# Performance work log

Measured on AMD Instinct MI355X. Metric: run time of the kernel, lower is better.

The kernel has to match this reference:

```python
import jax, jax.numpy as jnp
import numpy as np

B, S, H = 4, 2048, 1024
NH = 1                     # source code only type-checks with 1 head (see notes)
DH = H // NH               # head dim == hidden size
DT = 32                    # distance_type
LN_EPS = 1e-12


def setup_inputs() -> dict:
    key = jax.random.key(0)
    ks = jax.random.split(key, 12)
    sd = 0.02
    hidden_states = jax.random.normal(ks[0], (B, S, H), dtype=jnp.float32)
    attention_mask = jnp.zeros((B, 1, 1, S), dtype=jnp.float32)
    word_word_relation = jax.random.randint(ks[1], (B, S, S), 0, DT, dtype=jnp.int64)
    dist_emb = sd * jax.random.normal(ks[2], (DT, H), dtype=jnp.float32)
    dist_emb = dist_emb.at[0].set(0.0)  # padding_idx=0
    return {
        "hidden_states": hidden_states,
        "attention_mask": attention_mask,
        "word_word_relation": word_word_relation,
        "Wq": sd * jax.random.normal(ks[3], (H, H), dtype=jnp.float32),
        "bq": jnp.zeros((H,), dtype=jnp.float32),
        "Wk": sd * jax.random.normal(ks[4], (H, H), dtype=jnp.float32),
        "bk": jnp.zeros((H,), dtype=jnp.float32),
        "Wv": sd * jax.random.normal(ks[5], (H, H), dtype=jnp.float32),
        "bv": jnp.zeros((H,), dtype=jnp.float32),
        "dist_emb": dist_emb,
        "Wo": sd * jax.random.normal(ks[6], (H, H), dtype=jnp.float32),
        "bo": jnp.zeros((H,), dtype=jnp.float32),
        "ln_g": jnp.ones((H,), dtype=jnp.float32),
        "ln_b": jnp.zeros((H,), dtype=jnp.float32),
    }


def _split_heads(x):
    # [B,S,H] -> [B,NH,S,DH]
    return x.reshape(B, S, NH, DH).transpose(0, 2, 1, 3)


def reference(hidden_states, attention_mask, word_word_relation, Wq, bq, Wk, bk,
              Wv, bv, dist_emb, Wo, bo, ln_g, ln_b):
    q = _split_heads(hidden_states @ Wq.T + bq)   # [B,NH,S,DH]
    k = _split_heads(hidden_states @ Wk.T + bk)
    v = _split_heads(hidden_states @ Wv.T + bv)

    # raw QK^T scores [B,NH,S,S]
    scores = jnp.einsum('bhqd,bhkd->bhqk', q, k)

    # query . distance_embedding^T : [B,NH,S,DT]
    word_dot_distance = jnp.einsum('bhqd,td->bhqt', q, dist_emb)

    rel = word_word_relation[:, None, :, :]       # [B,1,S,S]
    # gather per-pair distance score along the distance-type axis
    dist_att = jnp.take_along_axis(word_dot_distance, rel, axis=3)  # [B,NH,S,S]
    mask_out = (rel == 1).astype(scores.dtype)    # keep only relation==1 pairs
    dist_att = dist_att * mask_out

    scores = (scores + dist_att) / jnp.sqrt(jnp.asarray(DH, scores.dtype))
    scores = scores + attention_mask              # additive BERT mask
    probs = jax.nn.softmax(scores, axis=-1)       # dropout p=0 -> identity

    ctx = jnp.einsum('bhqk,bhkd->bhqd', probs, v) # [B,NH,S,DH]
    ctx = ctx.transpose(0, 2, 1, 3).reshape(B, S, H)

    # BertSelfOutput: dense -> residual -> LayerNorm
    attn_out = ctx @ Wo.T + bo
    x = attn_out + hidden_states
    mu = jnp.mean(x, axis=-1, keepdims=True)
    var = jnp.mean(jnp.square(x - mu), axis=-1, keepdims=True)
    out = (x - mu) * jax.lax.rsqrt(var + LN_EPS) * ln_g + ln_b
    return out
```

## Files before the change

### kernel.cpp

```cpp
#include <hip/hip_runtime.h>

#define BM 256
#define BN 128
#define BK 64
#define NBUF 3
#define BUFELEMS ((BM + BN) * BK)

typedef __bf16 bf16x8 __attribute__((ext_vector_type(8)));
typedef __bf16 bf16x4 __attribute__((ext_vector_type(4)));
typedef float f32x4 __attribute__((ext_vector_type(4)));
typedef __bf16 bf16_t;

#define MFMA16(a, b, c) __builtin_amdgcn_mfma_f32_16x16x32_bf16((a), (b), (c), 0, 0, 0)

__device__ __forceinline__ void gl_lds16(const void* g, void* l) {
    __builtin_amdgcn_global_load_lds(
        (const __attribute__((address_space(1))) void*)g,
        (__attribute__((address_space(3))) void*)l, 16, 0, 0);
}
__device__ __forceinline__ void barrier_mem() {
    asm volatile("s_barrier" ::: "memory");
}

__global__ __launch_bounds__(256)
void cvt_all_kernel(const float* __restrict__ hid,
                    const float* __restrict__ w0, const float* __restrict__ w1,
                    const float* __restrict__ w2, const float* __restrict__ w3,
                    bf16_t* __restrict__ hidb, bf16_t* __restrict__ wb)
{
    const int bid = blockIdx.x;
    const float* src;
    bf16_t* dst;
    size_t off;
    if (bid < 8192) {
        src = hid; dst = hidb; off = (size_t)bid * 1024;
    } else {
        const int i = (bid - 8192) >> 10;
        src = (i == 0) ? w0 : (i == 1) ? w1 : (i == 2) ? w2 : w3;
        dst = wb + (size_t)i * 1024 * 1024;
        off = (size_t)((bid - 8192) & 1023) * 1024;
    }
    const size_t idx = off + threadIdx.x * 4;
    const float4 v = *(const float4*)(src + idx);
    bf16x4 o;
    o[0] = (__bf16)v.x; o[1] = (__bf16)v.y;
    o[2] = (__bf16)v.z; o[3] = (__bf16)v.w;
    *(bf16x4*)(dst + idx) = o;
}

template <int MODE>
__global__ __launch_bounds__(512, 2)
void gemm_bt(const bf16_t* __restrict__ A, const bf16_t* __restrict__ Bw,
             const float* __restrict__ bias, const float* __restrict__ bias2,
             const float* __restrict__ bias3,
             bf16_t* __restrict__ C, bf16_t* __restrict__ C2,
             int M, int N, int K,
             long long sAz, long long sBz, long long sCz,
             const float* __restrict__ resid,
             int Sdim, int DHdim)
{
    const int bz = blockIdx.z;
    const float* bi = bias;
    if (MODE == 0) {
        Bw += (long long)bz * N * K;
        bi = (bz == 0) ? bias : (bz == 1 ? bias2 : bias3);
        if (bz < 2) C += (long long)bz * sCz;
    } else {
        A += (long long)bz * sAz;
        Bw += (long long)bz * sBz;
        C += (long long)bz * sCz;
    }
    const int num_n = N / BN;
    const int pid = blockIdx.x;
    const int group = 8 * num_n;
    const int g = pid / group;
    const int m0 = (g * 8 + (pid % 8)) * BM;
    const int n0 = ((pid % group) >> 3) * BN;

    const int tid = threadIdx.x;
    const int w = tid >> 6;
    const int lane = tid & 63;
    const int wr = w >> 1;
    const int wc = w & 1;
    const int frow = lane & 15;
    const int fchunk = lane >> 4;

    __shared__ bf16_t smem[NBUF * BUFELEMS];

    const int srow8 = lane >> 3;
    const int sch = (lane & 7) ^ srow8;
    const size_t soff = (size_t)(w * 8 + srow8) * K + ((size_t)sch << 3);
    const bf16_t* gA = A + (size_t)m0 * K;
    const bf16_t* gB = Bw + (size_t)n0 * K;

    auto stA = [&](int kt, int b, int i) {
        gl_lds16(gA + (size_t)(i * 64) * K + (size_t)kt * BK + soff,
                 smem + (size_t)b * BUFELEMS + (i * 64 + w * 8) * BK);
    };
    auto stB = [&](int kt, int b, int i) {
        gl_lds16(gB + (size_t)(i * 64) * K + (size_t)kt * BK + soff,
                 smem + (size_t)b * BUFELEMS + BM * BK + (i * 64 + w * 8) * BK);
    };

    f32x4 acc[4][4];
#pragma unroll
    for (int i = 0; i < 4; ++i)
#pragma unroll
        for (int j = 0; j < 4; ++j) acc[i][j] = (f32x4)0.0f;

    const int NT = K / BK;

#pragma unroll
    for (int i = 0; i < 4; ++i) stA(0, 0, i);
#pragma unroll
    for (int i = 0; i < 2; ++i) stB(0, 0, i);
#pragma unroll
    for (int i = 0; i < 4; ++i) stA(1, 1, i);
#pragma unroll
    for (int i = 0; i < 2; ++i) stB(1, 1, i);

    for (int kt = 0; kt < NT; ++kt) {
        const int cur = kt % NBUF;
        const int nxt = (kt + 2) % NBUF;
        const bool pf = (kt + 2 < NT);
        if (pf) { stA(kt + 2, nxt, 0); stA(kt + 2, nxt, 1); stA(kt + 2, nxt, 2); }
        if (pf)               asm volatile("s_waitcnt vmcnt(9)" ::: "memory");
        else if (kt + 1 < NT) asm volatile("s_waitcnt vmcnt(6)" ::: "memory");
        else                  asm volatile("s_waitcnt vmcnt(0)" ::: "memory");
        barrier_mem();

        const bf16_t* Ab = smem + (size_t)cur * BUFELEMS;
        const bf16_t* Bb = Ab + BM * BK;
        const int sw = frow & 7;

        bf16x8 af[4][2], b0v[2][2];
#pragma unroll
        for (int t = 0; t < 4; ++t) {
            const int row = wr * 64 + t * 16 + frow;
#pragma unroll
            for (int kh = 0; kh < 2; ++kh)
                af[t][kh] = *(const bf16x8*)&Ab[row * BK + (((kh * 4 + fchunk) ^ sw) << 3)];
        }
#pragma unroll
        for (int u = 0; u < 2; ++u) {
            const int row = wc * 64 + u * 16 + frow;
#pragma unroll
            for (int kh = 0; kh < 2; ++kh)
                b0v[u][kh] = *(const bf16x8*)&Bb[row * BK + (((kh * 4 + fchunk) ^ sw) << 3)];
        }
        if (pf) { stA(kt + 2, nxt, 3); stB(kt + 2, nxt, 0); stB(kt + 2, nxt, 1); }

        __builtin_amdgcn_s_setprio(1);
#pragma unroll
        for (int t = 0; t < 4; ++t)
#pragma unroll
            for (int u = 0; u < 2; ++u) {
                acc[t][u] = MFMA16(af[t][0], b0v[u][0], acc[t][u]);
                acc[t][u] = MFMA16(af[t][1], b0v[u][1], acc[t][u]);
            }
        __builtin_amdgcn_s_setprio(0);

        bf16x8 b1v[2][2];
#pragma unroll
        for (int u = 0; u < 2; ++u) {
            const int row = wc * 64 + (u + 2) * 16 + frow;
#pragma unroll
            for (int kh = 0; kh < 2; ++kh)
                b1v[u][kh] = *(const bf16x8*)&Bb[row * BK + (((kh * 4 + fchunk) ^ sw) << 3)];
        }
        barrier_mem();

        __builtin_amdgcn_s_setprio(1);
#pragma unroll
        for (int t = 0; t < 4; ++t)
#pragma unroll
            for (int u = 0; u < 2; ++u) {
                acc[t][u + 2] = MFMA16(af[t][0], b1v[u][0], acc[t][u + 2]);
                acc[t][u + 2] = MFMA16(af[t][1], b1v[u][1], acc[t][u + 2]);
            }
        __builtin_amdgcn_s_setprio(0);
        barrier_mem();
    }

    const int crow = (lane >> 4) * 4;
    const int ccol = lane & 15;

    if (MODE == 0 && bz == 2) {
#pragma unroll
        for (int mt = 0; mt < 4; ++mt) {
            const int mb = m0 + wr * 64 + mt * 16 + crow;
#pragma unroll
            for (int nt = 0; nt < 4; ++nt) {
                const int n = n0 + wc * 64 + nt * 16 + ccol;
                const float bvv = bi[n];
                const int b = mb >> 11;
                const int s = mb & 2047;
                union { ushort4 u; bf16_t h[4]; } pk;
#pragma unroll
                for (int r = 0; r < 4; ++r) pk.h[r] = (__bf16)(acc[mt][nt][r] + bvv);
                *(ushort4*)&C2[(size_t)b * DHdim * Sdim + (size_t)n * Sdim + s] = pk.u;
            }
        }
        return;
    }

    bf16_t* tw = smem + w * (16 * 72);
    const int r0 = lane >> 3;
    const int cseg = (lane & 7) * 8;

    float bv[4];
    if (MODE == 0 || MODE == 4) {
#pragma unroll
        for (int nt = 0; nt < 4; ++nt)
            bv[nt] = bi[n0 + wc * 64 + nt * 16 + ccol];
    }

#pragma unroll
    for (int mt = 0; mt < 4; ++mt) {
#pragma unroll
        for (int nt = 0; nt < 4; ++nt) {
            const float badd = (MODE == 0 || MODE == 4) ? bv[nt] : 0.0f;
#pragma unroll
            for (int r = 0; r < 4; ++r)
                tw[(crow + r) * 72 + nt * 16 + ccol] = (__bf16)(acc[mt][nt][r] + badd);
        }
        bf16x8 va = *(const bf16x8*)&tw[r0 * 72 + cseg];
        bf16x8 vb = *(const bf16x8*)&tw[(r0 + 8) * 72 + cseg];

        const int gm_a = m0 + wr * 64 + mt * 16 + r0;
        const int gm_b = gm_a + 8;
        const int gn = n0 + wc * 64 + cseg;

        if (MODE == 0 || MODE == 3) {
            *(bf16x8*)&C[(size_t)gm_a * N + gn] = va;
            *(bf16x8*)&C[(size_t)gm_b * N + gn] = vb;
        } else {
            const float4 xa0 = *(const float4*)&resid[(size_t)gm_a * N + gn];
            const float4 xa1 = *(const float4*)&resid[(size_t)gm_a * N + gn + 4];
            const float4 xb0 = *(const float4*)&resid[(size_t)gm_b * N + gn];
            const float4 xb1 = *(const float4*)&resid[(size_t)gm_b * N + gn + 4];
            bf16x8 oa, ob;
            oa[0] = (__bf16)((float)va[0] + xa0.x);
            oa[1] = (__bf16)((float)va[1] + xa0.y);
            oa[2] = (__bf16)((float)va[2] + xa0.z);
            oa[3] = (__bf16)((float)va[3] + xa0.w);
            oa[4] = (__bf16)((float)va[4] + xa1.x);
            oa[5] = (__bf16)((float)va[5] + xa1.y);
            oa[6] = (__bf16)((float)va[6] + xa1.z);
            oa[7] = (__bf16)((float)va[7] + xa1.w);
            ob[0] = (__bf16)((float)vb[0] + xb0.x);
            ob[1] = (__bf16)((float)vb[1] + xb0.y);
            ob[2] = (__bf16)((float)vb[2] + xb0.z);
            ob[3] = (__bf16)((float)vb[3] + xb0.w);
            ob[4] = (__bf16)((float)vb[4] + xb1.x);
            ob[5] = (__bf16)((float)vb[5] + xb1.y);
            ob[6] = (__bf16)((float)vb[6] + xb1.z);
            ob[7] = (__bf16)((float)vb[7] + xb1.w);
            *(bf16x8*)&C[(size_t)gm_a * N + gn] = oa;
            *(bf16x8*)&C[(size_t)gm_b * N + gn] = ob;
        }
    }
}

__global__ __launch_bounds__(256)
void softmax_kernel(bf16_t* __restrict__ sc, const int* __restrict__ rel,
                    const bf16_t* __restrict__ q, const float* __restrict__ de,
                    const float* __restrict__ mask)
{
    constexpr int S = 2048, H = 1024;
    const int row = blockIdx.x;
    const int b = row >> 11;
    const int tid = threadIdx.x;
    const int w = tid >> 6, lane = tid & 63;
    __shared__ float rd1[4], rmax[4], rsum[4];

    const bf16x4 q4 = *(const bf16x4*)(q + (size_t)row * H + tid * 4);
    const float4 e4 = *(const float4*)(de + H + tid * 4);
    float pd = (float)q4[0] * e4.x + (float)q4[1] * e4.y
             + (float)q4[2] * e4.z + (float)q4[3] * e4.w;
#pragma unroll
    for (int off = 32; off; off >>= 1) pd += __shfl_xor(pd, off, 64);
    if (lane == 0) rd1[w] = pd;
    __syncthreads();
    const float d1s = (rd1[0] + rd1[1] + rd1[2] + rd1[3]) * 0.03125f;

    bf16_t* p = sc + (size_t)row * S;
    const bf16x8 x = *(const bf16x8*)(p + tid * 8);
    const int4 rl0 = *(const int4*)&rel[(size_t)row * S + tid * 8];
    const int4 rl1 = *(const int4*)&rel[(size_t)row * S + tid * 8 + 4];
    const float4 mk0 = *(const float4*)&mask[(size_t)b * S + tid * 8];
    const float4 mk1 = *(const float4*)&mask[(size_t)b * S + tid * 8 + 4];
    const int rls[8] = {rl0.x, rl0.y, rl0.z, rl0.w, rl1.x, rl1.y, rl1.z, rl1.w};
    const float mks[8] = {mk0.x, mk0.y, mk0.z, mk0.w, mk1.x, mk1.y, mk1.z, mk1.w};
    float v[8];
    float mx = -1e30f;
#pragma unroll
    for (int j = 0; j < 8; ++j) {
        v[j] = (float)x[j] * 0.03125f + mks[j] + (rls[j] == 1 ? d1s : 0.0f);
        mx = fmaxf(mx, v[j]);
    }
#pragma unroll
    for (int off = 32; off; off >>= 1) mx = fmaxf(mx, __shfl_xor(mx, off, 64));
    if (lane == 0) rmax[w] = mx;
    __syncthreads();
    mx = fmaxf(fmaxf(rmax[0], rmax[1]), fmaxf(rmax[2], rmax[3]));
    float sum = 0.0f;
#pragma unroll
    for (int j = 0; j < 8; ++j) { v[j] = __expf(v[j] - mx); sum += v[j]; }
#pragma unroll
    for (int off = 32; off; off >>= 1) sum += __shfl_xor(sum, off, 64);
    if (lane == 0) rsum[w] = sum;
    __syncthreads();
    sum = rsum[0] + rsum[1] + rsum[2] + rsum[3];
    const float inv = 1.0f / sum;
    bf16x8 o;
#pragma unroll
    for (int j = 0; j < 8; ++j) o[j] = (__bf16)(v[j] * inv);
    *(bf16x8*)(p + tid * 8) = o;
}

__global__ __launch_bounds__(256)
void ln_kernel(const bf16_t* __restrict__ x, const float* __restrict__ gamma,
               const float* __restrict__ beta, float* __restrict__ out)
{
    const int H = 1024;
    const size_t row = blockIdx.x;
    const int tid = threadIdx.x;
    const int w = tid >> 6, lane = tid & 63;
    bf16x4 xv = *(const bf16x4*)(x + row * H + tid * 4);
    float v[4] = {(float)xv[0], (float)xv[1], (float)xv[2], (float)xv[3]};
    float s = 0.0f, s2 = 0.0f;
#pragma unroll
    for (int j = 0; j < 4; ++j) { s += v[j]; s2 += v[j] * v[j]; }
#pragma unroll
    for (int off = 32; off; off >>= 1) {
        s += __shfl_xor(s, off, 64);
        s2 += __shfl_xor(s2, off, 64);
    }
    __shared__ float rs[4], rs2[4];
    if (lane == 0) { rs[w] = s; rs2[w] = s2; }
    __syncthreads();
    s  = rs[0] + rs[1] + rs[2] + rs[3];
    s2 = rs2[0] + rs2[1] + rs2[2] + rs2[3];
    const float mu  = s * (1.0f / H);
    const float var = s2 * (1.0f / H) - mu * mu;
    const float inv = rsqrtf(var + 1e-12f);
    float4 o;
    const int c = tid * 4;
    o.x = (v[0] - mu) * inv * gamma[c + 0] + beta[c + 0];
    o.y = (v[1] - mu) * inv * gamma[c + 1] + beta[c + 1];
    o.z = (v[2] - mu) * inv * gamma[c + 2] + beta[c + 2];
    o.w = (v[3] - mu) * inv * gamma[c + 3] + beta[c + 3];
    *(float4*)(out + row * H + tid * 4) = o;
}

extern "C" void kernel_launch(void* const* d_in, const int* in_sizes, int n_in,
                              void* d_out, int out_size, void* d_ws, size_t ws_size,
                              hipStream_t stream)
{
    constexpr int B = 4, S = 2048, H = 1024;
    const float* hid = (const float*)d_in[0];
    const float* am  = (const float*)d_in[1];
    const int*   rel = (const int*)d_in[2];
    const float* Wq  = (const float*)d_in[3];
    const float* bq  = (const float*)d_in[4];
    const float* Wk  = (const float*)d_in[5];
    const float* bk  = (const float*)d_in[6];
    const float* Wv  = (const float*)d_in[7];
    const float* bv  = (const float*)d_in[8];
    const float* de  = (const float*)d_in[9];
    const float* Wo  = (const float*)d_in[10];
    const float* bo  = (const float*)d_in[11];
    const float* lng = (const float*)d_in[12];
    const float* lnb = (const float*)d_in[13];
    float* out = (float*)d_out;

    char* ws = (char*)d_ws;
    const int n_tok = B * S;
    const size_t MB = 1024 * 1024;
    bf16_t* hidb = (bf16_t*)(ws);
    bf16_t* Wqb  = (bf16_t*)(ws + 16 * MB);
    bf16_t* Wob  = (bf16_t*)(ws + 22 * MB);
    bf16_t* qb   = (bf16_t*)(ws + 24 * MB);
    bf16_t* kb   = (bf16_t*)(ws + 40 * MB);
    bf16_t* vT   = (bf16_t*)(ws + 56 * MB);
    bf16_t* ctx  = (bf16_t*)(ws + 72 * MB);
    bf16_t* sc   = (bf16_t*)(ws + 88 * MB);
    bf16_t* xb   = (bf16_t*)(ws + 88 * MB);

    const dim3 blk(256);
    const dim3 blkg(512);
    cvt_all_kernel<<<dim3(8192 + 4 * 1024), blk, 0, stream>>>(
        hid, Wq, Wk, Wv, Wo, hidb, Wqb);

    gemm_bt<0><<<dim3((n_tok / BM) * (H / BN), 1, 3), blkg, 0, stream>>>(
        hidb, Wqb, bq, bk, bv, qb, vT, n_tok, H, H,
        0, 0, (long long)n_tok * H,
        nullptr, S, H);
    gemm_bt<3><<<dim3((S / BM) * (S / BN), 1, B), blkg, 0, stream>>>(
        qb, kb, nullptr, nullptr, nullptr, sc, nullptr, S, S, H,
        (long long)S * H, (long long)S * H, (long long)S * S,
        nullptr, S, H);
    softmax_kernel<<<dim3(B * S), blk, 0, stream>>>(sc, rel, qb, de, am);
    gemm_bt<3><<<dim3((S / BM) * (H / BN), 1, B), blkg, 0, stream>>>(
        sc, vT, nullptr, nullptr, nullptr, ctx, nullptr, S, H, S,
        (long long)S * S, (long long)H * S, (long long)S * H,
        nullptr, S, H);
    gemm_bt<4><<<dim3((n_tok / BM) * (H / BN), 1, 1), blkg, 0, stream>>>(
        ctx, Wob, bo, nullptr, nullptr, xb, nullptr, n_tok, H, H, 0, 0, 0,
        hid, S, H);
    ln_kernel<<<dim3(n_tok), blk, 0, stream>>>(xb, lng, lnb, out);
}
```

Measured before the change: 335.5 us.

## Add 256x256-tile GEMM with 8-phase LDS pipeline for QKV and QK^T

Adds a new gemm8 kernel with 256x256 output tiles, each wave computing 128x64, double-buffered A/B LDS halves, and an 8-phase schedule that interleaves global-to-LDS loads with MFMA work. It also uses grouped block ordering for L2 reuse. The QKV projection and the QK^T score GEMM now use gemm8, while the remaining gemm_bt calls get split A-fragment loads and have their unused MODE 0 paths removed. The larger tiles cut global traffic per FLOP and reduce the number of blocks. The cost is higher register pressure from 128 accumulator floats per lane and fewer blocks, which may hurt occupancy and tail balance.

```diff
diff --git a/kernel.cpp b/kernel.cpp
--- a/kernel.cpp
+++ b/kernel.cpp
@@ -46,6 +46,190 @@
     o[0] = (__bf16)v.x; o[1] = (__bf16)v.y;
     o[2] = (__bf16)v.z; o[3] = (__bf16)v.w;
     *(bf16x4*)(dst + idx) = o;
+}
+
+#define PHASE(BUF, P, SG, SL, VM)                                            \
+  do {                                                                       \
+    bf16x8 a00 = rdA(BUF, 2 * (P), 0),     a01 = rdA(BUF, 2 * (P), 1);       \
+    bf16x8 a10 = rdA(BUF, 2 * (P) + 1, 0), a11 = rdA(BUF, 2 * (P) + 1, 1);   \
+    if ((P) == 0) {                                                          \
+      _Pragma("unroll")                                                      \
+      for (int nf = 0; nf < 4; ++nf) {                                       \
+        bfrag[nf][0] = rdB(BUF, nf, 0);                                      \
+        bfrag[nf][1] = rdB(BUF, nf, 1);                                      \
+      }                                                                      \
+    }                                                                        \
+    if (SG) {                                                                \
+      gl_lds16((SG) + soff,                   (SL) + (w << 9));              \
+      gl_lds16((SG) + soff + (size_t)64 * K,  (SL) + 4096 + (w << 9));       \
+    }                                                                        \
+    barrier_mem();                                                           \
+    asm volatile("s_waitcnt lgkmcnt(0)" ::: "memory");                       \
+    __builtin_amdgcn_s_setprio(1);                                           \
+    _Pragma("unroll")                                                        \
+    for (int nf = 0; nf < 4; ++nf) {                                         \
+      acc[2 * (P)][nf]     = MFMA16(a00, bfrag[nf][0], acc[2 * (P)][nf]);    \
+      acc[2 * (P)][nf]     = MFMA16(a01, bfrag[nf][1], acc[2 * (P)][nf]);    \
+      acc[2 * (P) + 1][nf] = MFMA16(a10, bfrag[nf][0], acc[2 * (P) + 1][nf]);\
+      acc[2 * (P) + 1][nf] = MFMA16(a11, bfrag[nf][1], acc[2 * (P) + 1][nf]);\
+    }                                                                        \
+    __builtin_amdgcn_s_setprio(0);                                           \
+    if ((VM) == 4)      asm volatile("s_waitcnt vmcnt(4)" ::: "memory");     \
+    else if ((VM) == 0) asm volatile("s_waitcnt vmcnt(0)" ::: "memory");     \
+    barrier_mem();                                                           \
+  } while (0)
+
+template <int MODE>
+__global__ __launch_bounds__(512, 2)
+void gemm8(const bf16_t* __restrict__ A, const bf16_t* __restrict__ Bw,
+           const float* __restrict__ bias, const float* __restrict__ bias2,
+           const float* __restrict__ bias3,
+           bf16_t* __restrict__ C, bf16_t* __restrict__ C2,
+           int M, int N, int K,
+           long long sAz, long long sBz, long long sCz,
+           int Sdim, int DHdim)
+{
+    const int bz = blockIdx.z;
+    const float* bi = bias;
+    if (MODE == 0) {
+        Bw += (long long)bz * N * K;
+        bi = (bz == 0) ? bias : (bz == 1 ? bias2 : bias3);
+        if (bz < 2) C += (long long)bz * sCz;
+    } else {
+        A += (long long)bz * sAz;
+        Bw += (long long)bz * sBz;
+        C += (long long)bz * sCz;
+    }
+    const int num_n = N >> 8;
+    const int pid = blockIdx.x;
+    const int group = 8 * num_n;
+    const int g = pid / group;
+    const int m0 = (g * 8 + (pid % 8)) * 256;
+    const int n0 = ((pid % group) >> 3) * 256;
+
+    const int tid = threadIdx.x;
+    const int w = tid >> 6;
+    const int lane = tid & 63;
+    const int wr = w >> 2;
+    const int wc = w & 3;
+    const int frow = lane & 15;
+    const int fchunk = lane >> 4;
+
+    __shared__ bf16_t smem[4 * 16384];
+    bf16_t* A0b = smem;
+    bf16_t* A1b = smem + 16384;
+    bf16_t* B0b = smem + 32768;
+    bf16_t* B1b = smem + 49152;
+
+    const int srow = tid >> 3;
+    const int sch  = (tid & 7) ^ (srow & 7);
+    const size_t soff = (size_t)srow * K + ((size_t)sch << 3);
+
+    const bf16_t* gA = A + (size_t)m0 * K;
+    const bf16_t* gB = Bw + (size_t)n0 * K;
+
+    auto rdA = [&](int buf, int mf, int kh) -> bf16x8 {
+        const int row = wr * 128 + mf * 16 + frow;
+        return *(const bf16x8*)&smem[buf * 16384 + row * 64 +
+                                     (((kh * 4 + fchunk) ^ (frow & 7)) << 3)];
+    };
+    auto rdB = [&](int buf, int nf, int kh) -> bf16x8 {
+        const int row = wc * 64 + nf * 16 + frow;
+        return *(const bf16x8*)&smem[32768 + buf * 16384 + row * 64 +
+                                     (((kh * 4 + fchunk) ^ (frow & 7)) << 3)];
+    };
+    auto issue = [&](const bf16_t* sg, bf16_t* sl) {
+        gl_lds16(sg + soff,                  sl + (w << 9));
+        gl_lds16(sg + soff + (size_t)64 * K, sl + 4096 + (w << 9));
+    };
+
+    f32x4 acc[8][4];
+#pragma unroll
+    for (int i = 0; i < 8; ++i)
+#pragma unroll
+        for (int j = 0; j < 4; ++j) acc[i][j] = (f32x4)0.0f;
+    bf16x8 bfrag[4][2];
+
+    const int NT = K >> 6;
+    const int NI = NT >> 1;
+
+    issue(gB,                       B0b);
+    issue(gB + (size_t)128 * K,     B0b + 8192);
+    issue(gA,                       A0b);
+    issue(gA + (size_t)128 * K,     A0b + 8192);
+    issue(gB + 64,                  B1b);
+    issue(gB + 64 + (size_t)128 * K, B1b + 8192);
+    asm volatile("s_waitcnt vmcnt(4)" ::: "memory");
+    barrier_mem();
+
+    for (int it = 0; it < NI; ++it) {
+        const int t0 = 2 * it;
+        const bool pf = (t0 + 2) < NT;
+        const bf16_t* a1g = gA + (size_t)(t0 + 1) * 64;
+        const bf16_t* a2g = pf ? gA + (size_t)(t0 + 2) * 64 : nullptr;
+        const bf16_t* b2g = pf ? gB + (size_t)(t0 + 2) * 64 : nullptr;
+        const bf16_t* b3g = pf ? gB + (size_t)(t0 + 3) * 64 : nullptr;
+
+        PHASE(0, 0, a1g,                                      A1b,        -1);
+        PHASE(0, 1, a1g + (size_t)128 * K,                    A1b + 8192, -1);
+        PHASE(0, 2, b2g,                                      B0b,        -1);
+        PHASE(0, 3, (b2g ? b2g + (size_t)128 * K : nullptr),  B0b + 8192, (pf ? 4 : 0));
+        PHASE(1, 0, a2g,                                      A0b,        -1);
+        PHASE(1, 1, (a2g ? a2g + (size_t)128 * K : nullptr),  A0b + 8192, -1);
+        PHASE(1, 2, b3g,                                      B1b,        -1);
+        PHASE(1, 3, (b3g ? b3g + (size_t)128 * K : nullptr),  B1b + 8192, (pf ? 4 : -1));
+    }
+
+    const int crow = (lane >> 4) * 4;
+    const int ccol = lane & 15;
+
+    if (MODE == 0 && bz == 2) {
+#pragma unroll
+        for (int mt = 0; mt < 8; ++mt) {
+            const int mb = m0 + wr * 128 + mt * 16 + crow;
+#pragma unroll
+            for (int nt = 0; nt < 4; ++nt) {
+                const int n = n0 + wc * 64 + nt * 16 + ccol;
+                const float bvv = bi[n];
+                const int b = mb >> 11;
+                const int s = mb & 2047;
+                union { ushort4 u; bf16_t h[4]; } pk;
+#pragma unroll
+                for (int r = 0; r < 4; ++r) pk.h[r] = (__bf16)(acc[mt][nt][r] + bvv);
+                *(ushort4*)&C2[(size_t)b * DHdim * Sdim + (size_t)n * Sdim + s] = pk.u;
+            }
+        }
+        return;
+    }
+
+    bf16_t* tw = smem + w * (16 * 72);
+    const int r0 = lane >> 3;
+    const int cseg = (lane & 7) * 8;
+
+    float bv[4];
+    if (MODE == 0) {
+#pragma unroll
+        for (int nt = 0; nt < 4; ++nt)
+            bv[nt] = bi[n0 + wc * 64 + nt * 16 + ccol];
+    }
+
+#pragma unroll
+    for (int mt = 0; mt < 8; ++mt) {
+#pragma unroll
+        for (int nt = 0; nt < 4; ++nt) {
+            const float badd = (MODE == 0) ? bv[nt] : 0.0f;
+#pragma unroll
+            for (int r = 0; r < 4; ++r)
+                tw[(crow + r) * 72 + nt * 16 + ccol] = (__bf16)(acc[mt][nt][r] + badd);
+        }
+        bf16x8 va = *(const bf16x8*)&tw[r0 * 72 + cseg];
+        bf16x8 vb = *(const bf16x8*)&tw[(r0 + 8) * 72 + cseg];
+        const int gm_a = m0 + wr * 128 + mt * 16 + r0;
+        const int gm_b = gm_a + 8;
+        const int gn = n0 + wc * 64 + cseg;
+        *(bf16x8*)&C[(size_t)gm_a * N + gn] = va;
+        *(bf16x8*)&C[(size_t)gm_b * N + gn] = vb;
+    }
 }
 
 template <int MODE>
@@ -133,13 +317,17 @@
         const bf16_t* Bb = Ab + BM * BK;
         const int sw = frow & 7;
 
-        bf16x8 af[4][2], b0v[2][2];
+        bf16x8 af[4], b0v[2][2];
 #pragma unroll
         for (int t = 0; t < 4; ++t) {
             const int row = wr * 64 + t * 16 + frow;
-#pragma unroll
-            for (int kh = 0; kh < 2; ++kh)
-                af[t][kh] = *(const bf16x8*)&Ab[row * BK + (((kh * 4 + fchunk) ^ sw) << 3)];
+            af[t] = *(const bf16x8*)&Ab[row * BK + ((fchunk ^ sw) << 3)];
+        }
+        bf16x8 af1[4];
+#pragma unroll
+        for (int t = 0; t < 4; ++t) {
+            const int row = wr * 64 + t * 16 + frow;
+            af1[t] = *(const bf16x8*)&Ab[row * BK + (((4 + fchunk) ^ sw) << 3)];
         }
 #pragma unroll
         for (int u = 0; u < 2; ++u) {
@@ -155,8 +343,8 @@
         for (int t = 0; t < 4; ++t)
 #pragma unroll
             for (int u = 0; u < 2; ++u) {
-                acc[t][u] = MFMA16(af[t][0], b0v[u][0], acc[t][u]);
-                acc[t][u] = MFMA16(af[t][1], b0v[u][1], acc[t][u]);
+                acc[t][u] = MFMA16(af[t], b0v[u][0], acc[t][u]);
+                acc[t][u] = MFMA16(af1[t], b0v[u][1], acc[t][u]);
             }
         __builtin_amdgcn_s_setprio(0);
 
@@ -175,8 +363,8 @@
         for (int t = 0; t < 4; ++t)
 #pragma unroll
             for (int u = 0; u < 2; ++u) {
-                acc[t][u + 2] = MFMA16(af[t][0], b1v[u][0], acc[t][u + 2]);
-                acc[t][u + 2] = MFMA16(af[t][1], b1v[u][1], acc[t][u + 2]);
+                acc[t][u + 2] = MFMA16(af[t], b1v[u][0], acc[t][u + 2]);
+                acc[t][u + 2] = MFMA16(af1[t], b1v[u][1], acc[t][u + 2]);
             }
         __builtin_amdgcn_s_setprio(0);
         barrier_mem();
@@ -185,31 +373,12 @@
     const int crow = (lane >> 4) * 4;
     const int ccol = lane & 15;
 
-    if (MODE == 0 && bz == 2) {
-#pragma unroll
-        for (int mt = 0; mt < 4; ++mt) {
-            const int mb = m0 + wr * 64 + mt * 16 + crow;
-#pragma unroll
-            for (int nt = 0; nt < 4; ++nt) {
-                const int n = n0 + wc * 64 + nt * 16 + ccol;
-                const float bvv = bi[n];
-                const int b = mb >> 11;
-                const int s = mb & 2047;
-                union { ushort4 u; bf16_t h[4]; } pk;
-#pragma unroll
-                for (int r = 0; r < 4; ++r) pk.h[r] = (__bf16)(acc[mt][nt][r] + bvv);
-                *(ushort4*)&C2[(size_t)b * DHdim * Sdim + (size_t)n * Sdim + s] = pk.u;
-            }
-        }
-        return;
-    }
-
     bf16_t* tw = smem + w * (16 * 72);
     const int r0 = lane >> 3;
     const int cseg = (lane & 7) * 8;
 
     float bv[4];
-    if (MODE == 0 || MODE == 4) {
+    if (MODE == 4) {
 #pragma unroll
         for (int nt = 0; nt < 4; ++nt)
             bv[nt] = bi[n0 + wc * 64 + nt * 16 + ccol];
@@ -219,7 +388,7 @@
     for (int mt = 0; mt < 4; ++mt) {
 #pragma unroll
         for (int nt = 0; nt < 4; ++nt) {
-            const float badd = (MODE == 0 || MODE == 4) ? bv[nt] : 0.0f;
+            const float badd = (MODE == 4) ? bv[nt] : 0.0f;
 #pragma unroll
             for (int r = 0; r < 4; ++r)
                 tw[(crow + r) * 72 + nt * 16 + ccol] = (__bf16)(acc[mt][nt][r] + badd);
@@ -231,7 +400,7 @@
         const int gm_b = gm_a + 8;
         const int gn = n0 + wc * 64 + cseg;
 
-        if (MODE == 0 || MODE == 3) {
+        if (MODE == 3) {
             *(bf16x8*)&C[(size_t)gm_a * N + gn] = va;
             *(bf16x8*)&C[(size_t)gm_b * N + gn] = vb;
         } else {
@@ -393,14 +562,12 @@
     cvt_all_kernel<<<dim3(8192 + 4 * 1024), blk, 0, stream>>>(
         hid, Wq, Wk, Wv, Wo, hidb, Wqb);
 
-    gemm_bt<0><<<dim3((n_tok / BM) * (H / BN), 1, 3), blkg, 0, stream>>>(
+    gemm8<0><<<dim3(32 * 4, 1, 3), blkg, 0, stream>>>(
         hidb, Wqb, bq, bk, bv, qb, vT, n_tok, H, H,
-        0, 0, (long long)n_tok * H,
-        nullptr, S, H);
-    gemm_bt<3><<<dim3((S / BM) * (S / BN), 1, B), blkg, 0, stream>>>(
+        0, 0, (long long)n_tok * H, S, H);
+    gemm8<3><<<dim3(8 * 8, 1, B), blkg, 0, stream>>>(
         qb, kb, nullptr, nullptr, nullptr, sc, nullptr, S, S, H,
-        (long long)S * H, (long long)S * H, (long long)S * S,
-        nullptr, S, H);
+        (long long)S * H, (long long)S * H, (long long)S * S, S, H);
     softmax_kernel<<<dim3(B * S), blk, 0, stream>>>(sc, rel, qb, de, am);
     gemm_bt<3><<<dim3((S / BM) * (H / BN), 1, B), blkg, 0, stream>>>(
         sc, vT, nullptr, nullptr, nullptr, ctx, nullptr, S, H, S,
```

New measurement: 339.5 us. Within noise of the previous version (+1.2%).

## Add 128x128 BK32 double-buffered GEMM for the QKV projection

Applied to the files above, without the earlier changes.

Introduces a new gemm128 kernel with 128x128 output tiles, a K step of 32, two LDS buffers and 256 threads at occupancy 4, and uses it only for the fused QKV projection launch. The old 256x128 triple-buffered kernel remains for the other GEMMs. The intent is to give the QKV GEMM more, smaller blocks and higher occupancy, at the cost of less data reuse per tile and a shallower prefetch pipeline.

```diff
diff --git a/kernel.cpp b/kernel.cpp
--- a/kernel.cpp
+++ b/kernel.cpp
@@ -49,8 +49,8 @@
 }
 
 template <int MODE>
-__global__ __launch_bounds__(512, 2)
-void gemm_bt(const bf16_t* __restrict__ A, const bf16_t* __restrict__ Bw,
+__global__ __launch_bounds__(256, 4)
+void gemm128(const bf16_t* __restrict__ A, const bf16_t* __restrict__ Bw,
              const float* __restrict__ bias, const float* __restrict__ bias2,
              const float* __restrict__ bias3,
              bf16_t* __restrict__ C, bf16_t* __restrict__ C2,
@@ -70,12 +70,12 @@
         Bw += (long long)bz * sBz;
         C += (long long)bz * sCz;
     }
-    const int num_n = N / BN;
+    const int num_n = N >> 7;
     const int pid = blockIdx.x;
     const int group = 8 * num_n;
     const int g = pid / group;
-    const int m0 = (g * 8 + (pid % 8)) * BM;
-    const int n0 = ((pid % group) >> 3) * BN;
+    const int m0 = (g * 8 + (pid % 8)) * 128;
+    const int n0 = ((pid % group) >> 3) * 128;
 
     const int tid = threadIdx.x;
     const int w = tid >> 6;
@@ -85,22 +85,22 @@
     const int frow = lane & 15;
     const int fchunk = lane >> 4;
 
-    __shared__ bf16_t smem[NBUF * BUFELEMS];
-
-    const int srow8 = lane >> 3;
-    const int sch = (lane & 7) ^ srow8;
-    const size_t soff = (size_t)(w * 8 + srow8) * K + ((size_t)sch << 3);
+    __shared__ bf16_t smem[16384];
+
+    const size_t soff = (size_t)(tid >> 2) * K +
+                        ((size_t)((tid & 3) ^ ((tid >> 3) & 3)) << 3);
     const bf16_t* gA = A + (size_t)m0 * K;
     const bf16_t* gB = Bw + (size_t)n0 * K;
 
-    auto stA = [&](int kt, int b, int i) {
-        gl_lds16(gA + (size_t)(i * 64) * K + (size_t)kt * BK + soff,
-                 smem + (size_t)b * BUFELEMS + (i * 64 + w * 8) * BK);
+    auto stage = [&](int kt, int buf) {
+        const size_t ko = (size_t)kt * 32;
+        bf16_t* Ad = smem + buf * 4096;
+        bf16_t* Bd = smem + 8192 + buf * 4096;
+        gl_lds16(gA + ko + soff,                  Ad + (w << 9));
+        gl_lds16(gA + ko + soff + (size_t)64 * K, Ad + 2048 + (w << 9));
+        gl_lds16(gB + ko + soff,                  Bd + (w << 9));
+        gl_lds16(gB + ko + soff + (size_t)64 * K, Bd + 2048 + (w << 9));
     };
-    auto stB = [&](int kt, int b, int i) {
-        gl_lds16(gB + (size_t)(i * 64) * K + (size_t)kt * BK + soff,
-                 smem + (size_t)b * BUFELEMS + BM * BK + (i * 64 + w * 8) * BK);
-    };
 
     f32x4 acc[4][4];
 #pragma unroll
@@ -108,78 +108,37 @@
 #pragma unroll
         for (int j = 0; j < 4; ++j) acc[i][j] = (f32x4)0.0f;
 
-    const int NT = K / BK;
-
-#pragma unroll
-    for (int i = 0; i < 4; ++i) stA(0, 0, i);
-#pragma unroll
-    for (int i = 0; i < 2; ++i) stB(0, 0, i);
-#pragma unroll
-    for (int i = 0; i < 4; ++i) stA(1, 1, i);
-#pragma unroll
-    for (int i = 0; i < 2; ++i) stB(1, 1, i);
+    const int NT = K >> 5;
+    stage(0, 0);
+    stage(1, 1);
+    const int sw = (frow >> 1) & 3;
 
     for (int kt = 0; kt < NT; ++kt) {
-        const int cur = kt % NBUF;
-        const int nxt = (kt + 2) % NBUF;
-        const bool pf = (kt + 2 < NT);
-        if (pf) { stA(kt + 2, nxt, 0); stA(kt + 2, nxt, 1); stA(kt + 2, nxt, 2); }
-        if (pf)               asm volatile("s_waitcnt vmcnt(9)" ::: "memory");
-        else if (kt + 1 < NT) asm volatile("s_waitcnt vmcnt(6)" ::: "memory");
-        else                  asm volatile("s_waitcnt vmcnt(0)" ::: "memory");
+        const int buf = kt & 1;
+        if (kt + 1 < NT) asm volatile("s_waitcnt vmcnt(4)" ::: "memory");
+        else             asm volatile("s_waitcnt vmcnt(0)" ::: "memory");
         barrier_mem();
 
-        const bf16_t* Ab = smem + (size_t)cur * BUFELEMS;
-        const bf16_t* Bb = Ab + BM * BK;
-        const int sw = frow & 7;
-
-        bf16x8 af[4][2], b0v[2][2];
-#pragma unroll
-        for (int t = 0; t < 4; ++t) {
-            const int row = wr * 64 + t * 16 + frow;
-#pragma unroll
-            for (int kh = 0; kh < 2; ++kh)
-                af[t][kh] = *(const bf16x8*)&Ab[row * BK + (((kh * 4 + fchunk) ^ sw) << 3)];
-        }
-#pragma unroll
-        for (int u = 0; u < 2; ++u) {
-            const int row = wc * 64 + u * 16 + frow;
-#pragma unroll
-            for (int kh = 0; kh < 2; ++kh)
-                b0v[u][kh] = *(const bf16x8*)&Bb[row * BK + (((kh * 4 + fchunk) ^ sw) << 3)];
-        }
-        if (pf) { stA(kt + 2, nxt, 3); stB(kt + 2, nxt, 0); stB(kt + 2, nxt, 1); }
-
+        const bf16_t* Ab = smem + buf * 4096;
+        const bf16_t* Bb = smem + 8192 + buf * 4096;
+        bf16x8 af[4], bfv[4];
+#pragma unroll
+        for (int t = 0; t < 4; ++t)
+            af[t] = *(const bf16x8*)&Ab[(wr * 64 + t * 16 + frow) * 32 +
+                                        ((fchunk ^ sw) << 3)];
+#pragma unroll
+        for (int u = 0; u < 4; ++u)
+            bfv[u] = *(const bf16x8*)&Bb[(wc * 64 + u * 16 + frow) * 32 +
+                                         ((fchunk ^ sw) << 3)];
         __builtin_amdgcn_s_setprio(1);
 #pragma unroll
-        for (int t = 0; t < 4; ++t)
-#pragma unroll
-            for (int u = 0; u < 2; ++u) {
-                acc[t][u] = MFMA16(af[t][0], b0v[u][0], acc[t][u]);
-                acc[t][u] = MFMA16(af[t][1], b0v[u][1], acc[t][u]);
-            }
-        __builtin_amdgcn_s_setprio(0);
-
-        bf16x8 b1v[2][2];
-#pragma unroll
-        for (int u = 0; u < 2; ++u) {
-            const int row = wc * 64 + (u + 2) * 16 + frow;
-#pragma unroll
-            for (int kh = 0; kh < 2; ++kh)
-                b1v[u][kh] = *(const bf16x8*)&Bb[row * BK + (((kh * 4 + fchunk) ^ sw) << 3)];
-        }
-        barrier_mem();
-
-        __builtin_amdgcn_s_setprio(1);
-#pragma unroll
-        for (int t = 0; t < 4; ++t)
-#pragma unroll
-            for (int u = 0; u < 2; ++u) {
-                acc[t][u + 2] = MFMA16(af[t][0], b1v[u][0], acc[t][u + 2]);
-                acc[t][u + 2] = MFMA16(af[t][1], b1v[u][1], acc[t][u + 2]);
-            }
+        for (int mt = 0; mt < 4; ++mt)
+#pragma unroll
+            for (int nt = 0; nt < 4; ++nt)
+                acc[mt][nt] = MFMA16(af[mt], bfv[nt], acc[mt][nt]);
         __builtin_amdgcn_s_setprio(0);
         barrier_mem();
+        if (kt + 2 < NT) stage(kt + 2, buf);
     }
 
     const int crow = (lane >> 4) * 4;
@@ -226,7 +185,6 @@
         }
         bf16x8 va = *(const bf16x8*)&tw[r0 * 72 + cseg];
         bf16x8 vb = *(const bf16x8*)&tw[(r0 + 8) * 72 + cseg];
-
         const int gm_a = m0 + wr * 64 + mt * 16 + r0;
         const int gm_b = gm_a + 8;
         const int gn = n0 + wc * 64 + cseg;
@@ -262,6 +220,220 @@
     }
 }
 
+template <int MODE>
+__global__ __launch_bounds__(512, 2)
+void gemm_bt(const bf16_t* __restrict__ A, const bf16_t* __restrict__ Bw,
+             const float* __restrict__ bias, const float* __restrict__ bias2,
+             const float* __restrict__ bias3,
+             bf16_t* __restrict__ C, bf16_t* __restrict__ C2,
+             int M, int N, int K,
+             long long sAz, long long sBz, long long sCz,
+             const float* __restrict__ resid,
+             int Sdim, int DHdim)
+{
+    const int bz = blockIdx.z;
+    const float* bi = bias;
+    if (MODE == 0) {
+        Bw += (long long)bz * N * K;
+        bi = (bz == 0) ? bias : (bz == 1 ? bias2 : bias3);
+        if (bz < 2) C += (long long)bz * sCz;
+    } else {
+        A += (long long)bz * sAz;
+        Bw += (long long)bz * sBz;
+        C += (long long)bz * sCz;
+    }
+    const int num_n = N / BN;
+    const int pid = blockIdx.x;
+    const int group = 8 * num_n;
+    const int g = pid / group;
+    const int m0 = (g * 8 + (pid % 8)) * BM;
+    const int n0 = ((pid % group) >> 3) * BN;
+
+    const int tid = threadIdx.x;
+    const int w = tid >> 6;
+    const int lane = tid & 63;
+    const int wr = w >> 1;
+    const int wc = w & 1;
+    const int frow = lane & 15;
+    const int fchunk = lane >> 4;
+
+    __shared__ bf16_t smem[NBUF * BUFELEMS];
+
+    const int srow8 = lane >> 3;
+    const int sch = (lane & 7) ^ srow8;
+    const size_t soff = (size_t)(w * 8 + srow8) * K + ((size_t)sch << 3);
+    const bf16_t* gA = A + (size_t)m0 * K;
+    const bf16_t* gB = Bw + (size_t)n0 * K;
+
+    auto stA = [&](int kt, int b, int i) {
+        gl_lds16(gA + (size_t)(i * 64) * K + (size_t)kt * BK + soff,
+                 smem + (size_t)b * BUFELEMS + (i * 64 + w * 8) * BK);
+    };
+    auto stB = [&](int kt, int b, int i) {
+        gl_lds16(gB + (size_t)(i * 64) * K + (size_t)kt * BK + soff,
+                 smem + (size_t)b * BUFELEMS + BM * BK + (i * 64 + w * 8) * BK);
+    };
+
+    f32x4 acc[4][4];
+#pragma unroll
+    for (int i = 0; i < 4; ++i)
+#pragma unroll
+        for (int j = 0; j < 4; ++j) acc[i][j] = (f32x4)0.0f;
+
+    const int NT = K / BK;
+
+#pragma unroll
+    for (int i = 0; i < 4; ++i) stA(0, 0, i);
+#pragma unroll
+    for (int i = 0; i < 2; ++i) stB(0, 0, i);
+#pragma unroll
+    for (int i = 0; i < 4; ++i) stA(1, 1, i);
+#pragma unroll
+    for (int i = 0; i < 2; ++i) stB(1, 1, i);
+
+    for (int kt = 0; kt < NT; ++kt) {
+        const int cur = kt % NBUF;
+        const int nxt = (kt + 2) % NBUF;
+        const bool pf = (kt + 2 < NT);
+        if (pf) { stA(kt + 2, nxt, 0); stA(kt + 2, nxt, 1); stA(kt + 2, nxt, 2); }
+        if (pf)               asm volatile("s_waitcnt vmcnt(9)" ::: "memory");
+        else if (kt + 1 < NT) asm volatile("s_waitcnt vmcnt(6)" ::: "memory");
+        else                  asm volatile("s_waitcnt vmcnt(0)" ::: "memory");
+        barrier_mem();
+
+        const bf16_t* Ab = smem + (size_t)cur * BUFELEMS;
+        const bf16_t* Bb = Ab + BM * BK;
+        const int sw = frow & 7;
+
+        bf16x8 af[4][2], b0v[2][2];
+#pragma unroll
+        for (int t = 0; t < 4; ++t) {
+            const int row = wr * 64 + t * 16 + frow;
+#pragma unroll
+            for (int kh = 0; kh < 2; ++kh)
+                af[t][kh] = *(const bf16x8*)&Ab[row * BK + (((kh * 4 + fchunk) ^ sw) << 3)];
+        }
+#pragma unroll
+        for (int u = 0; u < 2; ++u) {
+            const int row = wc * 64 + u * 16 + frow;
+#pragma unroll
+            for (int kh = 0; kh < 2; ++kh)
+                b0v[u][kh] = *(const bf16x8*)&Bb[row * BK + (((kh * 4 + fchunk) ^ sw) << 3)];
+        }
+        if (pf) { stA(kt + 2, nxt, 3); stB(kt + 2, nxt, 0); stB(kt + 2, nxt, 1); }
+
+        __builtin_amdgcn_s_setprio(1);
+#pragma unroll
+        for (int t = 0; t < 4; ++t)
+#pragma unroll
+            for (int u = 0; u < 2; ++u) {
+                acc[t][u] = MFMA16(af[t][0], b0v[u][0], acc[t][u]);
+                acc[t][u] = MFMA16(af[t][1], b0v[u][1], acc[t][u]);
+            }
+        __builtin_amdgcn_s_setprio(0);
+
+        bf16x8 b1v[2][2];
+#pragma unroll
+        for (int u = 0; u < 2; ++u) {
+            const int row = wc * 64 + (u + 2) * 16 + frow;
+#pragma unroll
+            for (int kh = 0; kh < 2; ++kh)
+                b1v[u][kh] = *(const bf16x8*)&Bb[row * BK + (((kh * 4 + fchunk) ^ sw) << 3)];
+        }
+        barrier_mem();
+
+        __builtin_amdgcn_s_setprio(1);
+#pragma unroll
+        for (int t = 0; t < 4; ++t)
+#pragma unroll
+            for (int u = 0; u < 2; ++u) {
+                acc[t][u + 2] = MFMA16(af[t][0], b1v[u][0], acc[t][u + 2]);
+                acc[t][u + 2] = MFMA16(af[t][1], b1v[u][1], acc[t][u + 2]);
+            }
+        __builtin_amdgcn_s_setprio(0);
+        barrier_mem();
+    }
+
+    const int crow = (lane >> 4) * 4;
+    const int ccol = lane & 15;
+
+    if (MODE == 0 && bz == 2) {
+#pragma unroll
+        for (int mt = 0; mt < 4; ++mt) {
+            const int mb = m0 + wr * 64 + mt * 16 + crow;
+#pragma unroll
+            for (int nt = 0; nt < 4; ++nt) {
+                const int n = n0 + wc * 64 + nt * 16 + ccol;
+                const float bvv = bi[n];
+                const int b = mb >> 11;
+                const int s = mb & 2047;
+                union { ushort4 u; bf16_t h[4]; } pk;
+#pragma unroll
+                for (int r = 0; r < 4; ++r) pk.h[r] = (__bf16)(acc[mt][nt][r] + bvv);
+                *(ushort4*)&C2[(size_t)b * DHdim * Sdim + (size_t)n * Sdim + s] = pk.u;
+            }
+        }
+        return;
+    }
+
+    bf16_t* tw = smem + w * (16 * 72);
+    const int r0 = lane >> 3;
+    const int cseg = (lane & 7) * 8;
+
+    float bv[4];
+    if (MODE == 0 || MODE == 4) {
+#pragma unroll
+        for (int nt = 0; nt < 4; ++nt)
+            bv[nt] = bi[n0 + wc * 64 + nt * 16 + ccol];
+    }
+
+#pragma unroll
+    for (int mt = 0; mt < 4; ++mt) {
+#pragma unroll
+        for (int nt = 0; nt < 4; ++nt) {
+            const float badd = (MODE == 0 || MODE == 4) ? bv[nt] : 0.0f;
+#pragma unroll
+            for (int r = 0; r < 4; ++r)
+                tw[(crow + r) * 72 + nt * 16 + ccol] = (__bf16)(acc[mt][nt][r] + badd);
+        }
+        bf16x8 va = *(const bf16x8*)&tw[r0 * 72 + cseg];
+        bf16x8 vb = *(const bf16x8*)&tw[(r0 + 8) * 72 + cseg];
+
+        const int gm_a = m0 + wr * 64 + mt * 16 + r0;
+        const int gm_b = gm_a + 8;
+        const int gn = n0 + wc * 64 + cseg;
+
+        if (MODE == 0 || MODE == 3) {
+            *(bf16x8*)&C[(size_t)gm_a * N + gn] = va;
+            *(bf16x8*)&C[(size_t)gm_b * N + gn] = vb;
+        } else {
+            const float4 xa0 = *(const float4*)&resid[(size_t)gm_a * N + gn];
+            const float4 xa1 = *(const float4*)&resid[(size_t)gm_a * N + gn + 4];
+            const float4 xb0 = *(const float4*)&resid[(size_t)gm_b * N + gn];
+            const float4 xb1 = *(const float4*)&resid[(size_t)gm_b * N + gn + 4];
+            bf16x8 oa, ob;
+            oa[0] = (__bf16)((float)va[0] + xa0.x);
+            oa[1] = (__bf16)((float)va[1] + xa0.y);
+            oa[2] = (__bf16)((float)va[2] + xa0.z);
+            oa[3] = (__bf16)((float)va[3] + xa0.w);
+            oa[4] = (__bf16)((float)va[4] + xa1.x);
+            oa[5] = (__bf16)((float)va[5] + xa1.y);
+            oa[6] = (__bf16)((float)va[6] + xa1.z);
+            oa[7] = (__bf16)((float)va[7] + xa1.w);
+            ob[0] = (__bf16)((float)vb[0] + xb0.x);
+            ob[1] = (__bf16)((float)vb[1] + xb0.y);
+            ob[2] = (__bf16)((float)vb[2] + xb0.z);
+            ob[3] = (__bf16)((float)vb[3] + xb0.w);
+            ob[4] = (__bf16)((float)vb[4] + xb1.x);
+            ob[5] = (__bf16)((float)vb[5] + xb1.y);
+            ob[6] = (__bf16)((float)vb[6] + xb1.z);
+            ob[7] = (__bf16)((float)vb[7] + xb1.w);
+            *(bf16x8*)&C[(size_t)gm_a * N + gn] = oa;
+            *(bf16x8*)&C[(size_t)gm_b * N + gn] = ob;
+        }
+    }
+}
+
 __global__ __launch_bounds__(256)
 void softmax_kernel(bf16_t* __restrict__ sc, const int* __restrict__ rel,
                     const bf16_t* __restrict__ q, const float* __restrict__ de,
@@ -393,7 +565,7 @@
     cvt_all_kernel<<<dim3(8192 + 4 * 1024), blk, 0, stream>>>(
         hid, Wq, Wk, Wv, Wo, hidb, Wqb);
 
-    gemm_bt<0><<<dim3((n_tok / BM) * (H / BN), 1, 3), blkg, 0, stream>>>(
+    gemm128<0><<<dim3(64 * 8, 1, 3), blk, 0, stream>>>(
         hidb, Wqb, bq, bk, bv, qb, vT, n_tok, H, H,
         0, 0, (long long)n_tok * H,
         nullptr, S, H);
```

Result: slower. 342.4 us (+2.0%).
